# Kernel optimization log

Measured on AMD Instinct MI355X. Metric: run time of the kernel, lower is better.

Reference implementation:

```python
import jax, jax.numpy as jnp
import numpy as np

B, E, H, S, V = 64, 2048, 1024, 512, 32000


def _lin(key, fan_in, fan_out):
    kw, kb = jax.random.split(key)
    s = 1.0 / np.sqrt(fan_in)
    W = jax.random.uniform(kw, (fan_in, fan_out), jnp.float32, -s, s)
    b = jax.random.uniform(kb, (fan_out,), jnp.float32, -s, s)
    return W, b


def setup_inputs() -> dict:
    key = jax.random.key(0)
    ks = jax.random.split(key, 10)
    x = jax.random.normal(ks[0], (B, E), jnp.float32)
    h0 = jax.random.normal(ks[1], (B, H), jnp.float32)
    c0 = jax.random.normal(ks[2], (B, H), jnp.float32)
    sv_emb = jax.random.normal(ks[3], (B, S, H), jnp.float32)
    # multiplicative path: weight_mx (E->H), weight_mh (H->H)
    Wmx, bmx = _lin(ks[4], E, H)
    Wmh, bmh = _lin(ks[5], H, H)
    # fused gate matrices: [f, i, o, c_tilde], inputs x (E) and m (H)
    Wx, bx = _lin(ks[6], E, 4 * H)
    Wm, bm = _lin(ks[7], H, 4 * H)
    # output projection: cat(h, context) (2H) -> vocab
    Wout, bout = _lin(ks[8], 2 * H, V)
    return dict(x=x, h0=h0, c0=c0, sv_emb=sv_emb, Wmx=Wmx, bmx=bmx,
                Wmh=Wmh, bmh=bmh, Wx=Wx, bx=bx, Wm=Wm, bm=bm,
                Wout=Wout, bout=bout)


def reference(x, h0, c0, sv_emb, Wmx, bmx, Wmh, bmh, Wx, bx, Wm, bm, Wout, bout):
    Hd = h0.shape[-1]
    # multiplicative LSTM cell (single step)
    m = (x @ Wmx + bmx) * (h0 @ Wmh + bmh)              # [B,H]
    g = (x @ Wx + bx) + (m @ Wm + bm)                   # [B,4H]
    f = jax.nn.sigmoid(g[:, :Hd])
    i = jax.nn.sigmoid(g[:, Hd:2 * Hd])
    o = jax.nn.sigmoid(g[:, 2 * Hd:3 * Hd])
    c_tilda = jnp.tanh(g[:, 3 * Hd:])
    c = f * c0 + i * c_tilda                            # [B,H]
    h = o * jnp.tanh(c)                                 # [B,H]
    # dot-product attention over sv_emb (vectorized form of the python loop)
    scores = jnp.einsum('bd,bsd->bs', h, sv_emb)        # [B,S]
    attn = jax.nn.softmax(scores, axis=-1)
    context = jnp.einsum('bs,bsd->bd', attn, sv_emb)    # [B,H]
    logits = jnp.concatenate([h, context], axis=-1) @ Wout + bout  # [B,V]
    return logits
```

## Files before the change

kernel.cpp:

```cpp
#include <hip/hip_runtime.h>

#define B_ 64
#define E_ 2048
#define H_ 1024
#define S_ 512
#define V_ 32000
#define NSPLIT 8

typedef __bf16 bf16x8 __attribute__((ext_vector_type(8)));
typedef float f32x4 __attribute__((ext_vector_type(4)));

__device__ __forceinline__ f32x4 mfma16(bf16x8 a, bf16x8 b, f32x4 c) {
  return __builtin_amdgcn_mfma_f32_16x16x32_bf16(a, b, c, 0, 0, 0);
}

__device__ __forceinline__ bf16x8 cvt8(const float* __restrict__ p) {
  f32x4 a = *(const f32x4*)p;
  f32x4 b = *(const f32x4*)(p + 4);
  bf16x8 r;
#pragma unroll
  for (int j = 0; j < 4; ++j) { r[j] = (__bf16)a[j]; r[4 + j] = (__bf16)b[j]; }
  return r;
}

__device__ __forceinline__ bf16x8 load_bfrag(const float* __restrict__ W, int ldw, int k, int v) {
  const float* p = W + (size_t)k * ldw + v;
  bf16x8 r;
#pragma unroll
  for (int j = 0; j < 8; ++j) r[j] = (__bf16)p[(size_t)j * ldw];
  return r;
}

__global__ __launch_bounds__(256) void k_m_and_g1(
    const float* __restrict__ x, const float* __restrict__ h0,
    const float* __restrict__ Wmx, const float* __restrict__ bmx,
    const float* __restrict__ Wmh, const float* __restrict__ bmh,
    const float* __restrict__ Wx,
    __bf16* __restrict__ m_out, float* __restrict__ g1) {
  const int tid = threadIdx.x;
  const int wave = tid >> 6, lane = tid & 63;
  const int mi = lane & 15, ki = (lane >> 4) * 8;
  const int arow = wave * 16 + mi;
  const int blk = blockIdx.x;
  if (blk < H_ / 16) {
    const int v0 = blk * 16;
    f32x4 amx = {0.f, 0.f, 0.f, 0.f};
    f32x4 amh = {0.f, 0.f, 0.f, 0.f};
    for (int k = 0; k < E_; k += 32) {
      bf16x8 a = cvt8(x + (size_t)arow * E_ + k + ki);
      bf16x8 b = load_bfrag(Wmx, H_, k + ki, v0 + mi);
      amx = mfma16(a, b, amx);
    }
    for (int k = 0; k < H_; k += 32) {
      bf16x8 a = cvt8(h0 + (size_t)arow * H_ + k + ki);
      bf16x8 b = load_bfrag(Wmh, H_, k + ki, v0 + mi);
      amh = mfma16(a, b, amh);
    }
    const int col = v0 + (lane & 15);
    const float bxv = bmx[col], bhv = bmh[col];
#pragma unroll
    for (int r = 0; r < 4; ++r) {
      int row = wave * 16 + (lane >> 4) * 4 + r;
      m_out[(size_t)row * H_ + col] = (__bf16)((amx[r] + bxv) * (amh[r] + bhv));
    }
  } else {
    const int v0 = (blk - H_ / 16) * 16;
    f32x4 acc = {0.f, 0.f, 0.f, 0.f};
    for (int k = 0; k < E_; k += 32) {
      bf16x8 a = cvt8(x + (size_t)arow * E_ + k + ki);
      bf16x8 b = load_bfrag(Wx, 4 * H_, k + ki, v0 + mi);
      acc = mfma16(a, b, acc);
    }
    const int col = v0 + (lane & 15);
#pragma unroll
    for (int r = 0; r < 4; ++r) {
      int row = wave * 16 + (lane >> 4) * 4 + r;
      g1[(size_t)row * 4 * H_ + col] = acc[r];
    }
  }
}

__global__ __launch_bounds__(256) void k_g2(
    const __bf16* __restrict__ m_in, const float* __restrict__ Wm,
    float* __restrict__ g2) {
  const int tid = threadIdx.x;
  const int wave = tid >> 6, lane = tid & 63;
  const int mi = lane & 15, ki = (lane >> 4) * 8;
  const int arow = wave * 16 + mi;
  const int v0 = blockIdx.x * 16;
  f32x4 acc = {0.f, 0.f, 0.f, 0.f};
  for (int k = 0; k < H_; k += 32) {
    bf16x8 a = *(const bf16x8*)(m_in + (size_t)arow * H_ + k + ki);
    bf16x8 b = load_bfrag(Wm, 4 * H_, k + ki, v0 + mi);
    acc = mfma16(a, b, acc);
  }
  const int col = v0 + (lane & 15);
#pragma unroll
  for (int r = 0; r < 4; ++r) {
    int row = wave * 16 + (lane >> 4) * 4 + r;
    g2[(size_t)row * 4 * H_ + col] = acc[r];
  }
}

__global__ __launch_bounds__(256) void k_gates(
    const float* __restrict__ g1, const float* __restrict__ g2,
    const float* __restrict__ bx, const float* __restrict__ bm,
    const float* __restrict__ c0,
    float* __restrict__ h_f32, __bf16* __restrict__ Acat) {
  const int idx = blockIdx.x * blockDim.x + threadIdx.x;
  const int b = idx >> 10, j = idx & (H_ - 1);
  const size_t base = (size_t)b * 4 * H_ + j;
  float gf = g1[base] + g2[base] + bx[j] + bm[j];
  float gi = g1[base + H_] + g2[base + H_] + bx[j + H_] + bm[j + H_];
  float go = g1[base + 2 * H_] + g2[base + 2 * H_] + bx[j + 2 * H_] + bm[j + 2 * H_];
  float gc = g1[base + 3 * H_] + g2[base + 3 * H_] + bx[j + 3 * H_] + bm[j + 3 * H_];
  float f = 1.f / (1.f + __expf(-gf));
  float i = 1.f / (1.f + __expf(-gi));
  float o = 1.f / (1.f + __expf(-go));
  float ct = tanhf(gc);
  float c = f * c0[(size_t)b * H_ + j] + i * ct;
  float h = o * tanhf(c);
  h_f32[(size_t)b * H_ + j] = h;
  Acat[(size_t)b * 2 * H_ + j] = (__bf16)h;
}

__global__ __launch_bounds__(256) void k_attn_partial(
    const float* __restrict__ sv, const float* __restrict__ h_f32,
    float* __restrict__ ctxp, float* __restrict__ Mp, float* __restrict__ Lp) {
  const int b = blockIdx.x >> 3, split = blockIdx.x & (NSPLIT - 1);
  const int t = threadIdx.x;
  const int d0 = t * 4;
  float hr[4];
#pragma unroll
  for (int i = 0; i < 4; ++i) hr[i] = h_f32[(size_t)b * H_ + d0 + i];
  float M = -1e30f, L = 0.f;
  float cx[4] = {0.f, 0.f, 0.f, 0.f};
  __shared__ float red[2][4][4];
  const float* svb = sv + ((size_t)b * S_ + split * (S_ / NSPLIT)) * H_;
  for (int s4 = 0; s4 < S_ / NSPLIT; s4 += 4) {
    float sval[4][4];
    float part[4];
#pragma unroll
    for (int ss = 0; ss < 4; ++ss) {
      f32x4 v4 = *(const f32x4*)(svb + (size_t)(s4 + ss) * H_ + d0);
      float dot = 0.f;
#pragma unroll
      for (int i = 0; i < 4; ++i) {
        sval[ss][i] = v4[i];
        dot += hr[i] * v4[i];
      }
      part[ss] = dot;
    }
#pragma unroll
    for (int ss = 0; ss < 4; ++ss)
#pragma unroll
      for (int off = 32; off > 0; off >>= 1) part[ss] += __shfl_xor(part[ss], off);
    const int wv = t >> 6, ln = t & 63;
    const int buf = (s4 >> 2) & 1;
    if (ln == 0) {
#pragma unroll
      for (int ss = 0; ss < 4; ++ss) red[buf][wv][ss] = part[ss];
    }
    __syncthreads();
#pragma unroll
    for (int ss = 0; ss < 4; ++ss) {
      float score = red[buf][0][ss] + red[buf][1][ss] + red[buf][2][ss] + red[buf][3][ss];
      float nM = fmaxf(M, score);
      float al = __expf(M - nM);
      float w = __expf(score - nM);
      L = L * al + w;
#pragma unroll
      for (int i = 0; i < 4; ++i) cx[i] = cx[i] * al + w * sval[ss][i];
      M = nM;
    }
  }
  const int p = b * NSPLIT + split;
#pragma unroll
  for (int i = 0; i < 4; ++i) ctxp[(size_t)p * H_ + d0 + i] = cx[i];
  if (t == 0) { Mp[p] = M; Lp[p] = L; }
}

__global__ __launch_bounds__(256) void k_attn_combine(
    const float* __restrict__ ctxp, const float* __restrict__ Mp,
    const float* __restrict__ Lp, __bf16* __restrict__ Acat) {
  const int b = blockIdx.x;
  const int t = threadIdx.x;
  const int d0 = t * 4;
  float gM = -1e30f;
#pragma unroll
  for (int s = 0; s < NSPLIT; ++s) gM = fmaxf(gM, Mp[b * NSPLIT + s]);
  float w[NSPLIT];
  float T = 0.f;
#pragma unroll
  for (int s = 0; s < NSPLIT; ++s) {
    w[s] = __expf(Mp[b * NSPLIT + s] - gM);
    T += w[s] * Lp[b * NSPLIT + s];
  }
  const float inv = 1.f / T;
  float cx[4] = {0.f, 0.f, 0.f, 0.f};
#pragma unroll
  for (int s = 0; s < NSPLIT; ++s) {
#pragma unroll
    for (int i = 0; i < 4; ++i) cx[i] += w[s] * ctxp[(size_t)(b * NSPLIT + s) * H_ + d0 + i];
  }
#pragma unroll
  for (int i = 0; i < 4; ++i)
    Acat[(size_t)b * 2 * H_ + H_ + d0 + i] = (__bf16)(cx[i] * inv);
}

__global__ __launch_bounds__(256) void k_logits(
    const __bf16* __restrict__ Acat, const float* __restrict__ Wout,
    const float* __restrict__ bout, float* __restrict__ out) {
  const int tid = threadIdx.x;
  const int wave = tid >> 6, lane = tid & 63;
  const int mi = lane & 15, ki = (lane >> 4) * 8;
  const int v0 = blockIdx.x * 64 + wave * 16;
  f32x4 acc[4] = {};
  for (int k = 0; k < 2 * H_; k += 32) {
    bf16x8 bfr = load_bfrag(Wout, V_, k + ki, v0 + mi);
#pragma unroll
    for (int mt = 0; mt < 4; ++mt) {
      bf16x8 a = *(const bf16x8*)(Acat + (size_t)(mt * 16 + mi) * 2 * H_ + k + ki);
      acc[mt] = mfma16(a, bfr, acc[mt]);
    }
  }
  const int col = v0 + (lane & 15);
  const float bo = bout[col];
#pragma unroll
  for (int mt = 0; mt < 4; ++mt)
#pragma unroll
    for (int r = 0; r < 4; ++r) {
      int row = mt * 16 + (lane >> 4) * 4 + r;
      out[(size_t)row * V_ + col] = acc[mt][r] + bo;
    }
}

extern "C" void kernel_launch(void* const* d_in, const int* in_sizes, int n_in,
                              void* d_out, int out_size, void* d_ws, size_t ws_size,
                              hipStream_t stream) {
  const float* x    = (const float*)d_in[0];
  const float* h0   = (const float*)d_in[1];
  const float* c0   = (const float*)d_in[2];
  const float* sv   = (const float*)d_in[3];
  const float* Wmx  = (const float*)d_in[4];
  const float* bmx  = (const float*)d_in[5];
  const float* Wmh  = (const float*)d_in[6];
  const float* bmh  = (const float*)d_in[7];
  const float* Wx   = (const float*)d_in[8];
  const float* bx   = (const float*)d_in[9];
  const float* Wm   = (const float*)d_in[10];
  const float* bm   = (const float*)d_in[11];
  const float* Wout = (const float*)d_in[12];
  const float* bout = (const float*)d_in[13];
  float* out = (float*)d_out;

  char* ws = (char*)d_ws;
  size_t off = 0;
  __bf16* m_ws = (__bf16*)(ws + off); off += (size_t)B_ * H_ * 2;
  float* g1_ws = (float*)(ws + off);  off += (size_t)B_ * 4 * H_ * 4;
  float* g2_ws = (float*)(ws + off);  off += (size_t)B_ * 4 * H_ * 4;
  float* h_ws  = (float*)(ws + off);  off += (size_t)B_ * H_ * 4;
  __bf16* Acat = (__bf16*)(ws + off); off += (size_t)B_ * 2 * H_ * 2;
  float* ctxp  = (float*)(ws + off);  off += (size_t)B_ * NSPLIT * H_ * 4;
  float* Mp    = (float*)(ws + off);  off += (size_t)B_ * NSPLIT * 4;
  float* Lp    = (float*)(ws + off);  off += (size_t)B_ * NSPLIT * 4;

  k_m_and_g1<<<H_ / 16 + 4 * H_ / 16, 256, 0, stream>>>(x, h0, Wmx, bmx, Wmh, bmh, Wx,
                                                        m_ws, g1_ws);
  k_g2<<<4 * H_ / 16, 256, 0, stream>>>(m_ws, Wm, g2_ws);
  k_gates<<<(B_ * H_) / 256, 256, 0, stream>>>(g1_ws, g2_ws, bx, bm, c0, h_ws, Acat);
  k_attn_partial<<<B_ * NSPLIT, 256, 0, stream>>>(sv, h_ws, ctxp, Mp, Lp);
  k_attn_combine<<<B_, 256, 0, stream>>>(ctxp, Mp, Lp, Acat);
  k_logits<<<V_ / 64, 256, 0, stream>>>(Acat, Wout, bout, out);
}
```

Before: 586.1 us.

## Stage weight tiles through LDS with coalesced vector loads and prefetch in GEMMs

Replaces the strided per-element weight fragment loads (eight rows apart per lane) with coalesced float4 row loads that are converted to bf16 and transposed into a double-buffered LDS tile, with the next tile prefetched into registers. The gate GEMMs widen to 32 columns per block, and the logits GEMM uses the same LDS staging. A new prep kernel converts x and h0 to bf16 once instead of every block converting them again. This targets the uncoalesced global traffic on the large weight matrices, at the cost of an extra launch, more workspace, LDS use and barriers.

Result: faster. 571.2 us (-2.5%).

```diff
diff --git a/kernel.cpp b/kernel.cpp
--- a/kernel.cpp
+++ b/kernel.cpp
@@ -23,83 +23,120 @@
   return r;
 }
 
-__device__ __forceinline__ bf16x8 load_bfrag(const float* __restrict__ W, int ldw, int k, int v) {
-  const float* p = W + (size_t)k * ldw + v;
-  bf16x8 r;
-#pragma unroll
-  for (int j = 0; j < 8; ++j) r[j] = (__bf16)p[(size_t)j * ldw];
-  return r;
-}
-
-__global__ __launch_bounds__(256) void k_m_and_g1(
+__global__ __launch_bounds__(256) void k_prep(
     const float* __restrict__ x, const float* __restrict__ h0,
+    __bf16* __restrict__ xb, __bf16* __restrict__ h0b) {
+  int idx = (blockIdx.x * 256 + threadIdx.x) * 8;
+  const float* src;
+  __bf16* dst;
+  if (idx < B_ * E_) { src = x + idx; dst = xb + idx; }
+  else { int j = idx - B_ * E_; src = h0 + j; dst = h0b + j; }
+  bf16x8 v = cvt8(src);
+  *(bf16x8*)dst = v;
+}
+
+__device__ __forceinline__ void gemm32(
+    const __bf16* __restrict__ A, int lda,
+    const float* __restrict__ Bg, int ldb, int K,
+    __bf16 (*lt)[32][72], f32x4 acc[2]) {
+  const int tid = threadIdx.x;
+  const int wave = tid >> 6, lane = tid & 63;
+  const int mi = lane & 15, ki = (lane >> 4) * 8;
+  const int c16 = (wave & 1) * 16;
+  const int mh = (wave >> 1) * 32;
+  const int sk = tid >> 3;
+  const int sv = (tid & 7) * 4;
+  const int NT = K / 64;
+  f32x4 pf0 = *(const f32x4*)(Bg + (size_t)sk * ldb + sv);
+  f32x4 pf1 = *(const f32x4*)(Bg + (size_t)(sk + 32) * ldb + sv);
+  for (int t = 0; t < NT; ++t) {
+    __bf16(*L)[72] = lt[t & 1];
+#pragma unroll
+    for (int i = 0; i < 4; ++i) {
+      L[sv + i][sk] = (__bf16)pf0[i];
+      L[sv + i][32 + sk] = (__bf16)pf1[i];
+    }
+    __syncthreads();
+    if (t + 1 < NT) {
+      const float* nb = Bg + (size_t)(t + 1) * 64 * ldb;
+      pf0 = *(const f32x4*)(nb + (size_t)sk * ldb + sv);
+      pf1 = *(const f32x4*)(nb + (size_t)(sk + 32) * ldb + sv);
+    }
+    const __bf16* Ab = A + (size_t)t * 64 + ki;
+#pragma unroll
+    for (int kk = 0; kk < 2; ++kk) {
+      bf16x8 bfrag = *(const bf16x8*)(&L[c16 + mi][kk * 32 + ki]);
+#pragma unroll
+      for (int mt = 0; mt < 2; ++mt) {
+        bf16x8 a = *(const bf16x8*)(Ab + (size_t)(mh + mt * 16 + mi) * lda + kk * 32);
+        acc[mt] = mfma16(a, bfrag, acc[mt]);
+      }
+    }
+  }
+}
+
+__global__ __launch_bounds__(256) void k_m_g1(
+    const __bf16* __restrict__ xb, const __bf16* __restrict__ h0b,
     const float* __restrict__ Wmx, const float* __restrict__ bmx,
     const float* __restrict__ Wmh, const float* __restrict__ bmh,
     const float* __restrict__ Wx,
     __bf16* __restrict__ m_out, float* __restrict__ g1) {
+  __shared__ __bf16 lt[2][32][72];
   const int tid = threadIdx.x;
   const int wave = tid >> 6, lane = tid & 63;
-  const int mi = lane & 15, ki = (lane >> 4) * 8;
-  const int arow = wave * 16 + mi;
+  const int mi = lane & 15;
+  const int c16 = (wave & 1) * 16;
+  const int mh = (wave >> 1) * 32;
   const int blk = blockIdx.x;
-  if (blk < H_ / 16) {
-    const int v0 = blk * 16;
-    f32x4 amx = {0.f, 0.f, 0.f, 0.f};
-    f32x4 amh = {0.f, 0.f, 0.f, 0.f};
-    for (int k = 0; k < E_; k += 32) {
-      bf16x8 a = cvt8(x + (size_t)arow * E_ + k + ki);
-      bf16x8 b = load_bfrag(Wmx, H_, k + ki, v0 + mi);
-      amx = mfma16(a, b, amx);
-    }
-    for (int k = 0; k < H_; k += 32) {
-      bf16x8 a = cvt8(h0 + (size_t)arow * H_ + k + ki);
-      bf16x8 b = load_bfrag(Wmh, H_, k + ki, v0 + mi);
-      amh = mfma16(a, b, amh);
-    }
-    const int col = v0 + (lane & 15);
+  if (blk < H_ / 32) {
+    const int v0 = blk * 32;
+    f32x4 amx[2] = {}, amh[2] = {};
+    gemm32(xb, E_, Wmx + v0, H_, E_, lt, amx);
+    gemm32(h0b, H_, Wmh + v0, H_, H_, lt, amh);
+    const int col = v0 + c16 + mi;
     const float bxv = bmx[col], bhv = bmh[col];
 #pragma unroll
-    for (int r = 0; r < 4; ++r) {
-      int row = wave * 16 + (lane >> 4) * 4 + r;
-      m_out[(size_t)row * H_ + col] = (__bf16)((amx[r] + bxv) * (amh[r] + bhv));
-    }
+    for (int mt = 0; mt < 2; ++mt)
+#pragma unroll
+      for (int r = 0; r < 4; ++r) {
+        int row = mh + mt * 16 + (lane >> 4) * 4 + r;
+        m_out[(size_t)row * H_ + col] = (__bf16)((amx[mt][r] + bxv) * (amh[mt][r] + bhv));
+      }
   } else {
-    const int v0 = (blk - H_ / 16) * 16;
-    f32x4 acc = {0.f, 0.f, 0.f, 0.f};
-    for (int k = 0; k < E_; k += 32) {
-      bf16x8 a = cvt8(x + (size_t)arow * E_ + k + ki);
-      bf16x8 b = load_bfrag(Wx, 4 * H_, k + ki, v0 + mi);
-      acc = mfma16(a, b, acc);
-    }
-    const int col = v0 + (lane & 15);
-#pragma unroll
-    for (int r = 0; r < 4; ++r) {
-      int row = wave * 16 + (lane >> 4) * 4 + r;
-      g1[(size_t)row * 4 * H_ + col] = acc[r];
-    }
+    const int v0 = (blk - H_ / 32) * 32;
+    f32x4 acc[2] = {};
+    gemm32(xb, E_, Wx + v0, 4 * H_, E_, lt, acc);
+    const int col = v0 + c16 + mi;
+#pragma unroll
+    for (int mt = 0; mt < 2; ++mt)
+#pragma unroll
+      for (int r = 0; r < 4; ++r) {
+        int row = mh + mt * 16 + (lane >> 4) * 4 + r;
+        g1[(size_t)row * 4 * H_ + col] = acc[mt][r];
+      }
   }
 }
 
 __global__ __launch_bounds__(256) void k_g2(
     const __bf16* __restrict__ m_in, const float* __restrict__ Wm,
     float* __restrict__ g2) {
+  __shared__ __bf16 lt[2][32][72];
   const int tid = threadIdx.x;
   const int wave = tid >> 6, lane = tid & 63;
-  const int mi = lane & 15, ki = (lane >> 4) * 8;
-  const int arow = wave * 16 + mi;
-  const int v0 = blockIdx.x * 16;
-  f32x4 acc = {0.f, 0.f, 0.f, 0.f};
-  for (int k = 0; k < H_; k += 32) {
-    bf16x8 a = *(const bf16x8*)(m_in + (size_t)arow * H_ + k + ki);
-    bf16x8 b = load_bfrag(Wm, 4 * H_, k + ki, v0 + mi);
-    acc = mfma16(a, b, acc);
-  }
-  const int col = v0 + (lane & 15);
-#pragma unroll
-  for (int r = 0; r < 4; ++r) {
-    int row = wave * 16 + (lane >> 4) * 4 + r;
-    g2[(size_t)row * 4 * H_ + col] = acc[r];
-  }
+  const int mi = lane & 15;
+  const int c16 = (wave & 1) * 16;
+  const int mh = (wave >> 1) * 32;
+  const int v0 = blockIdx.x * 32;
+  f32x4 acc[2] = {};
+  gemm32(m_in, H_, Wm + v0, 4 * H_, H_, lt, acc);
+  const int col = v0 + c16 + mi;
+#pragma unroll
+  for (int mt = 0; mt < 2; ++mt)
+#pragma unroll
+    for (int r = 0; r < 4; ++r) {
+      int row = mh + mt * 16 + (lane >> 4) * 4 + r;
+      g2[(size_t)row * 4 * H_ + col] = acc[mt][r];
+    }
 }
 
 __global__ __launch_bounds__(256) void k_gates(
@@ -211,20 +248,46 @@
 __global__ __launch_bounds__(256) void k_logits(
     const __bf16* __restrict__ Acat, const float* __restrict__ Wout,
     const float* __restrict__ bout, float* __restrict__ out) {
+  __shared__ __bf16 lt[2][64][72];
   const int tid = threadIdx.x;
   const int wave = tid >> 6, lane = tid & 63;
   const int mi = lane & 15, ki = (lane >> 4) * 8;
-  const int v0 = blockIdx.x * 64 + wave * 16;
+  const int v0 = blockIdx.x * 64;
+  const int sk = tid >> 4;
+  const int sv = (tid & 15) * 4;
+  const float* Bg = Wout + v0;
+  f32x4 pf[4];
+#pragma unroll
+  for (int r = 0; r < 4; ++r)
+    pf[r] = *(const f32x4*)(Bg + (size_t)(r * 16 + sk) * V_ + sv);
   f32x4 acc[4] = {};
-  for (int k = 0; k < 2 * H_; k += 32) {
-    bf16x8 bfr = load_bfrag(Wout, V_, k + ki, v0 + mi);
-#pragma unroll
-    for (int mt = 0; mt < 4; ++mt) {
-      bf16x8 a = *(const bf16x8*)(Acat + (size_t)(mt * 16 + mi) * 2 * H_ + k + ki);
-      acc[mt] = mfma16(a, bfr, acc[mt]);
-    }
-  }
-  const int col = v0 + (lane & 15);
+  const int NT = 2 * H_ / 64;
+  for (int t = 0; t < NT; ++t) {
+    __bf16(*L)[72] = lt[t & 1];
+#pragma unroll
+    for (int r = 0; r < 4; ++r)
+#pragma unroll
+      for (int i = 0; i < 4; ++i)
+        L[sv + i][r * 16 + sk] = (__bf16)pf[r][i];
+    __syncthreads();
+    if (t + 1 < NT) {
+      const float* nb = Bg + (size_t)(t + 1) * 64 * V_;
+#pragma unroll
+      for (int r = 0; r < 4; ++r)
+        pf[r] = *(const f32x4*)(nb + (size_t)(r * 16 + sk) * V_ + sv);
+    }
+    const __bf16* Ab = Acat + t * 64 + ki;
+#pragma unroll
+    for (int kk = 0; kk < 2; ++kk) {
+      bf16x8 bfrag = *(const bf16x8*)(&L[wave * 16 + mi][kk * 32 + ki]);
+#pragma unroll
+      for (int mt = 0; mt < 4; ++mt) {
+        bf16x8 a = *(const bf16x8*)(Ab + (size_t)(mt * 16 + mi) * 2 * H_ + kk * 32);
+        acc[mt] = mfma16(a, bfrag, acc[mt]);
+      }
+    }
+  }
+  const int col = v0 + wave * 16 + mi;
   const float bo = bout[col];
 #pragma unroll
   for (int mt = 0; mt < 4; ++mt)
@@ -264,10 +327,13 @@
   float* ctxp  = (float*)(ws + off);  off += (size_t)B_ * NSPLIT * H_ * 4;
   float* Mp    = (float*)(ws + off);  off += (size_t)B_ * NSPLIT * 4;
   float* Lp    = (float*)(ws + off);  off += (size_t)B_ * NSPLIT * 4;
-
-  k_m_and_g1<<<H_ / 16 + 4 * H_ / 16, 256, 0, stream>>>(x, h0, Wmx, bmx, Wmh, bmh, Wx,
-                                                        m_ws, g1_ws);
-  k_g2<<<4 * H_ / 16, 256, 0, stream>>>(m_ws, Wm, g2_ws);
+  __bf16* xb   = (__bf16*)(ws + off); off += (size_t)B_ * E_ * 2;
+  __bf16* h0b  = (__bf16*)(ws + off); off += (size_t)B_ * H_ * 2;
+
+  k_prep<<<(B_ * E_ + B_ * H_) / (256 * 8), 256, 0, stream>>>(x, h0, xb, h0b);
+  k_m_g1<<<H_ / 32 + 4 * H_ / 32, 256, 0, stream>>>(xb, h0b, Wmx, bmx, Wmh, bmh, Wx,
+                                                    m_ws, g1_ws);
+  k_g2<<<4 * H_ / 32, 256, 0, stream>>>(m_ws, Wm, g2_ws);
   k_gates<<<(B_ * H_) / 256, 256, 0, stream>>>(g1_ws, g2_ws, bx, bm, c0, h_ws, Acat);
   k_attn_partial<<<B_ * NSPLIT, 256, 0, stream>>>(sv, h_ws, ctxp, Mp, Lp);
   k_attn_combine<<<B_, 256, 0, stream>>>(ctxp, Mp, Lp, Acat);
```

## Stage weight tiles through LDS with coalesced loads and register prefetch

Applied to the files above, without the earlier changes.

Replaces the strided per-element weight fragment loads in all GEMM kernels with coalesced float4 row loads. These are converted to bf16, transposed into double-buffered LDS tiles, and prefetched one tile ahead in registers. Adds a prep kernel that converts x and h0 to bf16 once, so the GEMM blocks stop redoing the conversion, and adds register prefetch of sv rows in the attention partial kernel. The aim is to remove uncoalesced global reads of Wout, Wx, Wmx and Wm, at the cost of extra LDS traffic, barriers and one more launch.

Result: faster. 524.0 us (-10.6%).

```diff
diff --git a/kernel.cpp b/kernel.cpp
--- a/kernel.cpp
+++ b/kernel.cpp
@@ -6,12 +6,23 @@
 #define S_ 512
 #define V_ 32000
 #define NSPLIT 8
+#define KT 128
+#define LDT 136
+#define KT2 64
+#define LDT2 72
 
 typedef __bf16 bf16x8 __attribute__((ext_vector_type(8)));
 typedef float f32x4 __attribute__((ext_vector_type(4)));
+typedef unsigned int u32;
 
 __device__ __forceinline__ f32x4 mfma16(bf16x8 a, bf16x8 b, f32x4 c) {
   return __builtin_amdgcn_mfma_f32_16x16x32_bf16(a, b, c, 0, 0, 0);
+}
+
+__device__ __forceinline__ u32 packbf2(float lo, float hi) {
+  union { __bf16 h[2]; u32 w; } u;
+  u.h[0] = (__bf16)lo; u.h[1] = (__bf16)hi;
+  return u.w;
 }
 
 __device__ __forceinline__ bf16x8 cvt8(const float* __restrict__ p) {
@@ -23,40 +34,83 @@
   return r;
 }
 
-__device__ __forceinline__ bf16x8 load_bfrag(const float* __restrict__ W, int ldw, int k, int v) {
-  const float* p = W + (size_t)k * ldw + v;
-  bf16x8 r;
-#pragma unroll
-  for (int j = 0; j < 8; ++j) r[j] = (__bf16)p[(size_t)j * ldw];
-  return r;
-}
-
-__global__ __launch_bounds__(256) void k_m_and_g1(
+__global__ __launch_bounds__(256) void k_prep(
     const float* __restrict__ x, const float* __restrict__ h0,
+    __bf16* __restrict__ xb, __bf16* __restrict__ h0b) {
+  int idx = (blockIdx.x * 256 + threadIdx.x) * 8;
+  const float* src;
+  __bf16* dst;
+  if (idx < B_ * E_) { src = x + idx; dst = xb + idx; }
+  else { int j = idx - B_ * E_; src = h0 + j; dst = h0b + j; }
+  bf16x8 v = cvt8(src);
+  *(bf16x8*)dst = v;
+}
+
+__device__ __forceinline__ void gemm16(
+    const __bf16* __restrict__ A, int lda,
+    const float* __restrict__ Bg, int ldb, int K,
+    __bf16 (*At)[64][LDT], __bf16 (*Bt)[16][LDT], f32x4& acc) {
+  const int tid = threadIdx.x;
+  const int wave = tid >> 6, lane = tid & 63;
+  const int mi = lane & 15, ki = (lane >> 4) * 8;
+  const int bsv = (tid & 3) * 4;
+  const int bsk = (tid >> 2) * 2;
+  const int ar = tid >> 2;
+  const int ac = (tid & 3) * 32;
+  const int NT = K / KT;
+  f32x4 pB0 = *(const f32x4*)(Bg + (size_t)bsk * ldb + bsv);
+  f32x4 pB1 = *(const f32x4*)(Bg + (size_t)(bsk + 1) * ldb + bsv);
+  bf16x8 pA[4];
+#pragma unroll
+  for (int j = 0; j < 4; ++j)
+    pA[j] = *(const bf16x8*)(A + (size_t)ar * lda + ac + j * 8);
+  for (int t = 0; t < NT; ++t) {
+    __bf16(*LB)[LDT] = Bt[t & 1];
+    __bf16(*LA)[LDT] = At[t & 1];
+    u32* BW = (u32*)&LB[0][0];
+#pragma unroll
+    for (int i = 0; i < 4; ++i)
+      BW[(bsv + i) * (LDT / 2) + (bsk >> 1)] = packbf2(pB0[i], pB1[i]);
+#pragma unroll
+    for (int j = 0; j < 4; ++j)
+      *(bf16x8*)(&LA[ar][ac + j * 8]) = pA[j];
+    __syncthreads();
+    if (t + 1 < NT) {
+      const float* nB = Bg + (size_t)(t + 1) * KT * ldb;
+      pB0 = *(const f32x4*)(nB + (size_t)bsk * ldb + bsv);
+      pB1 = *(const f32x4*)(nB + (size_t)(bsk + 1) * ldb + bsv);
+      const __bf16* nA = A + (size_t)(t + 1) * KT;
+#pragma unroll
+      for (int j = 0; j < 4; ++j)
+        pA[j] = *(const bf16x8*)(nA + (size_t)ar * lda + ac + j * 8);
+    }
+#pragma unroll
+    for (int kk = 0; kk < 4; ++kk) {
+      bf16x8 bfrag = *(const bf16x8*)(&LB[mi][kk * 32 + ki]);
+      bf16x8 afrag = *(const bf16x8*)(&LA[wave * 16 + mi][kk * 32 + ki]);
+      acc = mfma16(afrag, bfrag, acc);
+    }
+  }
+}
+
+__global__ __launch_bounds__(256) void k_m_g1(
+    const __bf16* __restrict__ xb, const __bf16* __restrict__ h0b,
     const float* __restrict__ Wmx, const float* __restrict__ bmx,
     const float* __restrict__ Wmh, const float* __restrict__ bmh,
     const float* __restrict__ Wx,
     __bf16* __restrict__ m_out, float* __restrict__ g1) {
+  __shared__ __bf16 At[2][64][LDT];
+  __shared__ __bf16 Bt[2][16][LDT];
   const int tid = threadIdx.x;
   const int wave = tid >> 6, lane = tid & 63;
-  const int mi = lane & 15, ki = (lane >> 4) * 8;
-  const int arow = wave * 16 + mi;
+  const int mi = lane & 15;
   const int blk = blockIdx.x;
   if (blk < H_ / 16) {
     const int v0 = blk * 16;
-    f32x4 amx = {0.f, 0.f, 0.f, 0.f};
-    f32x4 amh = {0.f, 0.f, 0.f, 0.f};
-    for (int k = 0; k < E_; k += 32) {
-      bf16x8 a = cvt8(x + (size_t)arow * E_ + k + ki);
-      bf16x8 b = load_bfrag(Wmx, H_, k + ki, v0 + mi);
-      amx = mfma16(a, b, amx);
-    }
-    for (int k = 0; k < H_; k += 32) {
-      bf16x8 a = cvt8(h0 + (size_t)arow * H_ + k + ki);
-      bf16x8 b = load_bfrag(Wmh, H_, k + ki, v0 + mi);
-      amh = mfma16(a, b, amh);
-    }
-    const int col = v0 + (lane & 15);
+    f32x4 amx = {0.f, 0.f, 0.f, 0.f}, amh = {0.f, 0.f, 0.f, 0.f};
+    gemm16(xb, E_, Wmx + v0, H_, E_, At, Bt, amx);
+    gemm16(h0b, H_, Wmh + v0, H_, H_, At, Bt, amh);
+    const int col = v0 + mi;
     const float bxv = bmx[col], bhv = bmh[col];
 #pragma unroll
     for (int r = 0; r < 4; ++r) {
@@ -66,12 +120,8 @@
   } else {
     const int v0 = (blk - H_ / 16) * 16;
     f32x4 acc = {0.f, 0.f, 0.f, 0.f};
-    for (int k = 0; k < E_; k += 32) {
-      bf16x8 a = cvt8(x + (size_t)arow * E_ + k + ki);
-      bf16x8 b = load_bfrag(Wx, 4 * H_, k + ki, v0 + mi);
-      acc = mfma16(a, b, acc);
-    }
-    const int col = v0 + (lane & 15);
+    gemm16(xb, E_, Wx + v0, 4 * H_, E_, At, Bt, acc);
+    const int col = v0 + mi;
 #pragma unroll
     for (int r = 0; r < 4; ++r) {
       int row = wave * 16 + (lane >> 4) * 4 + r;
@@ -83,18 +133,15 @@
 __global__ __launch_bounds__(256) void k_g2(
     const __bf16* __restrict__ m_in, const float* __restrict__ Wm,
     float* __restrict__ g2) {
+  __shared__ __bf16 At[2][64][LDT];
+  __shared__ __bf16 Bt[2][16][LDT];
   const int tid = threadIdx.x;
   const int wave = tid >> 6, lane = tid & 63;
-  const int mi = lane & 15, ki = (lane >> 4) * 8;
-  const int arow = wave * 16 + mi;
+  const int mi = lane & 15;
   const int v0 = blockIdx.x * 16;
   f32x4 acc = {0.f, 0.f, 0.f, 0.f};
-  for (int k = 0; k < H_; k += 32) {
-    bf16x8 a = *(const bf16x8*)(m_in + (size_t)arow * H_ + k + ki);
-    bf16x8 b = load_bfrag(Wm, 4 * H_, k + ki, v0 + mi);
-    acc = mfma16(a, b, acc);
-  }
-  const int col = v0 + (lane & 15);
+  gemm16(m_in, H_, Wm + v0, 4 * H_, H_, At, Bt, acc);
+  const int col = v0 + mi;
 #pragma unroll
   for (int r = 0; r < 4; ++r) {
     int row = wave * 16 + (lane >> 4) * 4 + r;
@@ -124,6 +171,17 @@
   Acat[(size_t)b * 2 * H_ + j] = (__bf16)h;
 }
 
+__device__ __forceinline__ void sm_step(float score, const f32x4& cv,
+                                        float& M, float& L, float* cx) {
+  float nM = fmaxf(M, score);
+  float al = __expf(M - nM);
+  float w = __expf(score - nM);
+  L = L * al + w;
+#pragma unroll
+  for (int i = 0; i < 4; ++i) cx[i] = cx[i] * al + w * cv[i];
+  M = nM;
+}
+
 __global__ __launch_bounds__(256) void k_attn_partial(
     const float* __restrict__ sv, const float* __restrict__ h_f32,
     float* __restrict__ ctxp, float* __restrict__ Mp, float* __restrict__ Lp) {
@@ -136,21 +194,26 @@
   float M = -1e30f, L = 0.f;
   float cx[4] = {0.f, 0.f, 0.f, 0.f};
   __shared__ float red[2][4][4];
-  const float* svb = sv + ((size_t)b * S_ + split * (S_ / NSPLIT)) * H_;
-  for (int s4 = 0; s4 < S_ / NSPLIT; s4 += 4) {
-    float sval[4][4];
+  const int SB = S_ / NSPLIT;
+  const float* svb = sv + ((size_t)b * S_ + (size_t)split * SB) * H_;
+  f32x4 n0 = *(const f32x4*)(svb + (size_t)0 * H_ + d0);
+  f32x4 n1 = *(const f32x4*)(svb + (size_t)1 * H_ + d0);
+  f32x4 n2 = *(const f32x4*)(svb + (size_t)2 * H_ + d0);
+  f32x4 n3 = *(const f32x4*)(svb + (size_t)3 * H_ + d0);
+  for (int s4 = 0; s4 < SB; s4 += 4) {
+    f32x4 c0v = n0, c1v = n1, c2v = n2, c3v = n3;
+    if (s4 + 4 < SB) {
+      const float* p = svb + (size_t)(s4 + 4) * H_ + d0;
+      n0 = *(const f32x4*)(p);
+      n1 = *(const f32x4*)(p + H_);
+      n2 = *(const f32x4*)(p + 2 * H_);
+      n3 = *(const f32x4*)(p + 3 * H_);
+    }
     float part[4];
-#pragma unroll
-    for (int ss = 0; ss < 4; ++ss) {
-      f32x4 v4 = *(const f32x4*)(svb + (size_t)(s4 + ss) * H_ + d0);
-      float dot = 0.f;
-#pragma unroll
-      for (int i = 0; i < 4; ++i) {
-        sval[ss][i] = v4[i];
-        dot += hr[i] * v4[i];
-      }
-      part[ss] = dot;
-    }
+    part[0] = hr[0] * c0v[0] + hr[1] * c0v[1] + hr[2] * c0v[2] + hr[3] * c0v[3];
+    part[1] = hr[0] * c1v[0] + hr[1] * c1v[1] + hr[2] * c1v[2] + hr[3] * c1v[3];
+    part[2] = hr[0] * c2v[0] + hr[1] * c2v[1] + hr[2] * c2v[2] + hr[3] * c2v[3];
+    part[3] = hr[0] * c3v[0] + hr[1] * c3v[1] + hr[2] * c3v[2] + hr[3] * c3v[3];
 #pragma unroll
     for (int ss = 0; ss < 4; ++ss)
 #pragma unroll
@@ -162,17 +225,10 @@
       for (int ss = 0; ss < 4; ++ss) red[buf][wv][ss] = part[ss];
     }
     __syncthreads();
-#pragma unroll
-    for (int ss = 0; ss < 4; ++ss) {
-      float score = red[buf][0][ss] + red[buf][1][ss] + red[buf][2][ss] + red[buf][3][ss];
-      float nM = fmaxf(M, score);
-      float al = __expf(M - nM);
-      float w = __expf(score - nM);
-      L = L * al + w;
-#pragma unroll
-      for (int i = 0; i < 4; ++i) cx[i] = cx[i] * al + w * sval[ss][i];
-      M = nM;
-    }
+    sm_step(red[buf][0][0] + red[buf][1][0] + red[buf][2][0] + red[buf][3][0], c0v, M, L, cx);
+    sm_step(red[buf][0][1] + red[buf][1][1] + red[buf][2][1] + red[buf][3][1], c1v, M, L, cx);
+    sm_step(red[buf][0][2] + red[buf][1][2] + red[buf][2][2] + red[buf][3][2], c2v, M, L, cx);
+    sm_step(red[buf][0][3] + red[buf][1][3] + red[buf][2][3] + red[buf][3][3], c3v, M, L, cx);
   }
   const int p = b * NSPLIT + split;
 #pragma unroll
@@ -211,20 +267,66 @@
 __global__ __launch_bounds__(256) void k_logits(
     const __bf16* __restrict__ Acat, const float* __restrict__ Wout,
     const float* __restrict__ bout, float* __restrict__ out) {
+  __shared__ __bf16 At[2][64][LDT2];
+  __shared__ __bf16 Bt[2][64][LDT2];
   const int tid = threadIdx.x;
   const int wave = tid >> 6, lane = tid & 63;
   const int mi = lane & 15, ki = (lane >> 4) * 8;
-  const int v0 = blockIdx.x * 64 + wave * 16;
+  const int v0 = blockIdx.x * 64;
+  const int bsv = (tid & 15) * 4;
+  const int bsk = (tid >> 4) * 2;
+  const int ar = tid >> 2;
+  const int ac = (tid & 3) * 16;
+  const float* Bg = Wout + v0;
+  const int NT = 2 * H_ / KT2;
+  f32x4 pB[2][2];
+#pragma unroll
+  for (int r = 0; r < 2; ++r)
+#pragma unroll
+    for (int p = 0; p < 2; ++p)
+      pB[r][p] = *(const f32x4*)(Bg + (size_t)(bsk + 32 * r + p) * V_ + bsv);
+  bf16x8 pA[2];
+#pragma unroll
+  for (int j = 0; j < 2; ++j)
+    pA[j] = *(const bf16x8*)(Acat + (size_t)ar * 2 * H_ + ac + j * 8);
   f32x4 acc[4] = {};
-  for (int k = 0; k < 2 * H_; k += 32) {
-    bf16x8 bfr = load_bfrag(Wout, V_, k + ki, v0 + mi);
-#pragma unroll
-    for (int mt = 0; mt < 4; ++mt) {
-      bf16x8 a = *(const bf16x8*)(Acat + (size_t)(mt * 16 + mi) * 2 * H_ + k + ki);
-      acc[mt] = mfma16(a, bfr, acc[mt]);
-    }
-  }
-  const int col = v0 + (lane & 15);
+  for (int t = 0; t < NT; ++t) {
+    __bf16(*LB)[LDT2] = Bt[t & 1];
+    __bf16(*LA)[LDT2] = At[t & 1];
+    u32* BW = (u32*)&LB[0][0];
+#pragma unroll
+    for (int r = 0; r < 2; ++r)
+#pragma unroll
+      for (int i = 0; i < 4; ++i)
+        BW[(bsv + i) * (LDT2 / 2) + ((bsk + 32 * r) >> 1)] =
+            packbf2(pB[r][0][i], pB[r][1][i]);
+#pragma unroll
+    for (int j = 0; j < 2; ++j)
+      *(bf16x8*)(&LA[ar][ac + j * 8]) = pA[j];
+    __syncthreads();
+    if (t + 1 < NT) {
+      const float* nB = Bg + (size_t)(t + 1) * KT2 * V_;
+#pragma unroll
+      for (int r = 0; r < 2; ++r)
+#pragma unroll
+        for (int p = 0; p < 2; ++p)
+          pB[r][p] = *(const f32x4*)(nB + (size_t)(bsk + 32 * r + p) * V_ + bsv);
+      const __bf16* nA = Acat + (size_t)(t + 1) * KT2;
+#pragma unroll
+      for (int j = 0; j < 2; ++j)
+        pA[j] = *(const bf16x8*)(nA + (size_t)ar * 2 * H_ + ac + j * 8);
+    }
+#pragma unroll
+    for (int kk = 0; kk < 2; ++kk) {
+      bf16x8 bfrag = *(const bf16x8*)(&LB[wave * 16 + mi][kk * 32 + ki]);
+#pragma unroll
+      for (int mt = 0; mt < 4; ++mt) {
+        bf16x8 afrag = *(const bf16x8*)(&LA[mt * 16 + mi][kk * 32 + ki]);
+        acc[mt] = mfma16(afrag, bfrag, acc[mt]);
+      }
+    }
+  }
+  const int col = v0 + wave * 16 + mi;
   const float bo = bout[col];
 #pragma unroll
   for (int mt = 0; mt < 4; ++mt)
@@ -264,9 +366,12 @@
   float* ctxp  = (float*)(ws + off);  off += (size_t)B_ * NSPLIT * H_ * 4;
   float* Mp    = (float*)(ws + off);  off += (size_t)B_ * NSPLIT * 4;
   float* Lp    = (float*)(ws + off);  off += (size_t)B_ * NSPLIT * 4;
-
-  k_m_and_g1<<<H_ / 16 + 4 * H_ / 16, 256, 0, stream>>>(x, h0, Wmx, bmx, Wmh, bmh, Wx,
-                                                        m_ws, g1_ws);
+  __bf16* xb   = (__bf16*)(ws + off); off += (size_t)B_ * E_ * 2;
+  __bf16* h0b  = (__bf16*)(ws + off); off += (size_t)B_ * H_ * 2;
+
+  k_prep<<<(B_ * E_ + B_ * H_) / (256 * 8), 256, 0, stream>>>(x, h0, xb, h0b);
+  k_m_g1<<<H_ / 16 + 4 * H_ / 16, 256, 0, stream>>>(xb, h0b, Wmx, bmx, Wmh, bmh, Wx,
+                                                    m_ws, g1_ws);
   k_g2<<<4 * H_ / 16, 256, 0, stream>>>(m_ws, Wm, g2_ws);
   k_gates<<<(B_ * H_) / 256, 256, 0, stream>>>(g1_ws, g2_ws, bx, bm, c0, h_ws, Acat);
   k_attn_partial<<<B_ * NSPLIT, 256, 0, stream>>>(sv, h_ws, ctxp, Mp, Lp);
```
